# Performance work log

Hardware: AMD Instinct MI355X
Metric: run time of the kernel (lower is better)

The kernel has to match this reference:

```python
import jax, jax.numpy as jnp
import numpy as np
from math import factorial

IRREPS_IN1 = [(128, 0), (64, 1), (32, 2)]  # (mul, l): features
IRREPS_IN2 = [(1, 0), (1, 1), (1, 2)]      # spherical harmonics lmax=2
BATCH = 16384

# ---------- real Clebsch-Gordan coefficients (e3nn convention) ----------

def _su2_cg(j1, j2, j3, m1, m2, m3):
    if m3 != m1 + m2:
        return 0.0
    f = factorial
    pref = ((2 * j3 + 1) * f(j1 + j2 - j3) * f(j1 - j2 + j3) * f(-j1 + j2 + j3) / f(j1 + j2 + j3 + 1)) ** 0.5
    pref *= (f(j3 + m3) * f(j3 - m3) * f(j1 - m1) * f(j1 + m1) * f(j2 - m2) * f(j2 + m2)) ** 0.5
    s = 0.0
    for v in range(0, j1 + j2 - j3 + 1):
        a = j1 + j2 - j3 - v; b = j1 - m1 - v; c = j2 + m2 - v
        d = j3 - j2 + m1 + v; e = j3 - j1 - m2 + v
        if min(a, b, c, d, e) < 0:
            continue
        s += (-1) ** v / (f(v) * f(a) * f(b) * f(c) * f(d) * f(e))
    return pref * s


def _su2_cg_tensor(l1, l2, l3):
    C = np.zeros((2 * l1 + 1, 2 * l2 + 1, 2 * l3 + 1))
    for m1 in range(-l1, l1 + 1):
        for m2 in range(-l2, l2 + 1):
            for m3 in range(-l3, l3 + 1):
                C[l1 + m1, l2 + m2, l3 + m3] = _su2_cg(l1, l2, l3, m1, m2, m3)
    return C


def _q(l):
    # change of basis real -> complex spherical harmonics
    q = np.zeros((2 * l + 1, 2 * l + 1), dtype=np.complex128)
    for m in range(-l, 0):
        q[l + m, l + abs(m)] = 1.0 / np.sqrt(2.0)
        q[l + m, l - abs(m)] = -1j / np.sqrt(2.0)
    q[l, l] = 1.0
    for m in range(1, l + 1):
        q[l + m, l + abs(m)] = (-1) ** m / np.sqrt(2.0)
        q[l + m, l - abs(m)] = 1j * (-1) ** m / np.sqrt(2.0)
    return (-1j) ** l * q


def _real_cg(l1, l2, l3):
    C = _su2_cg_tensor(l1, l2, l3).astype(np.complex128)
    Q1, Q2, Q3 = _q(l1), _q(l2), _q(l3)
    C = np.einsum('ij,kl,mn,ikn->jlm', Q1, Q2, np.conj(Q3.T), C)
    assert np.abs(C.imag).max() < 1e-8
    return np.ascontiguousarray(C.real.astype(np.float32))

# precompute all CG tensors needed by the full tensor product
CG = {}
for _m1, _l1 in IRREPS_IN1:
    for _m2, _l2 in IRREPS_IN2:
        for _l3 in range(abs(_l1 - _l2), _l1 + _l2 + 1):
            if (_l1, _l2, _l3) not in CG:
                CG[(_l1, _l2, _l3)] = _real_cg(_l1, _l2, _l3)


def _tensor_product(x, y):
    """Full CG tensor product. x:[B,480] y:[B,9] -> dict l3 -> list of [B,mul,2l3+1]."""
    B = x.shape[0]
    outs = {}
    off1 = 0
    for mul1, l1 in IRREPS_IN1:
        d1 = 2 * l1 + 1
        x_blk = x[:, off1:off1 + mul1 * d1].reshape(B, mul1, d1)
        off1 += mul1 * d1
        off2 = 0
        for mul2, l2 in IRREPS_IN2:
            d2 = 2 * l2 + 1
            y_blk = y[:, off2:off2 + mul2 * d2].reshape(B, mul2, d2)
            off2 += mul2 * d2
            for l3 in range(abs(l1 - l2), l1 + l2 + 1):
                cg = jnp.asarray(CG[(l1, l2, l3)])  # [d1,d2,d3]
                z = jnp.einsum('ijk,bui,bvj->buvk', cg, x_blk, y_blk)
                outs.setdefault(l3, []).append(z.reshape(B, mul1 * mul2, 2 * l3 + 1))
    return outs


def setup_inputs() -> dict:
    key = jax.random.key(0)
    k = jax.random.split(key, 5)
    dim1 = sum(m * (2 * l + 1) for m, l in IRREPS_IN1)  # 480
    dim2 = sum(m * (2 * l + 1) for m, l in IRREPS_IN2)  # 9
    x = jax.random.normal(k[0], (BATCH, dim1), dtype=jnp.float32)
    y = jax.random.normal(k[1], (BATCH, dim2), dtype=jnp.float32)
    # fan-in per output l of the equivariant Linear (tp outputs with matching l)
    W0 = jax.random.normal(k[2], (224, 128), dtype=jnp.float32)
    W1 = jax.random.normal(k[3], (384, 64), dtype=jnp.float32)
    W2 = jax.random.normal(k[4], (352, 32), dtype=jnp.float32)
    return {"x": x, "y": y, "W0": W0, "W1": W1, "W2": W2}


def reference(x, y, W0, W1, W2):
    B = x.shape[0]
    outs = _tensor_product(x, y)
    Ws = {0: W0, 1: W1, 2: W2}
    res = []
    for mul_out, l in IRREPS_IN1:
        blk = jnp.concatenate(outs[l], axis=1)  # [B, tot_mul, 2l+1]
        tot_mul = blk.shape[1]
        o = jnp.einsum('bui,uv->bvi', blk, Ws[l]) / np.sqrt(tot_mul).astype(np.float32)
        res.append(o.reshape(B, mul_out * (2 * l + 1)))
    return jnp.concatenate(res, axis=1)  # [B, 480]
```

## Files before the change

kernel.cpp:

```cpp
#include <hip/hip_runtime.h>
#include <math.h>
#include <stdint.h>

#define NBATCH 16384
#define MB 16
#define NT 256
#define NBLOCKS (NBATCH/MB)
#define WT_BYTE_OFF 2560

typedef float  f32x4 __attribute__((ext_vector_type(4)));
typedef short  s16x8 __attribute__((ext_vector_type(8)));

constexpr double cfact(int n){ double r=1.0; for(int i=2;i<=n;++i) r*=(double)i; return r; }
constexpr double csqrt_(double x){
  if (x<=0.0) return 0.0;
  double m=x, k=1.0;
  while (m>1.0) { m*=0.25; k*=2.0; }
  while (m<0.25){ m*=4.0;  k*=0.5; }
  double g=0.7;
  for(int i=0;i<14;++i) g = 0.5*(g + m/g);
  return g*k;
}
constexpr double su2d(int j1,int j2,int j3,int m1,int m2,int m3){
  if (m1+m2 != m3) return 0.0;
  double pref = csqrt_((double)(2*j3+1)*cfact(j1+j2-j3)*cfact(j1-j2+j3)*cfact(-j1+j2+j3)/cfact(j1+j2+j3+1));
  pref *= csqrt_(cfact(j3+m3)*cfact(j3-m3)*cfact(j1-m1)*cfact(j1+m1)*cfact(j2-m2)*cfact(j2+m2));
  double s=0.0;
  for (int v=0; v<=j1+j2-j3; ++v){
    int a=j1+j2-j3-v, b=j1-m1-v, c=j2+m2-v, d=j3-j2+m1+v, e=j3-j1-m2+v;
    if (a<0||b<0||c<0||d<0||e<0) continue;
    double t = 1.0/(cfact(v)*cfact(a)*cfact(b)*cfact(c)*cfact(d)*cfact(e));
    s += (v&1)? -t : t;
  }
  return pref*s;
}
struct C2 { double re, im; };
constexpr C2 qvald(int l,int r,int c){
  int m = r - l;
  const double is2 = 0.70710678118654752440;
  double br=0.0, bi=0.0;
  if (m<0){ if (c==l-m) br=is2; else if (c==l+m) bi=-is2; }
  else if (m==0){ if (c==l) br=1.0; }
  else { double sg=(m&1)?-1.0:1.0; if (c==l+m) br=sg*is2; else if (c==l-m) bi=sg*is2; }
  if (l==1){ double nr=bi, ni=-br; br=nr; bi=ni; }
  else if (l==2){ br=-br; bi=-bi; }
  return C2{br,bi};
}
constexpr int HP_L1[15]={0,1,2,0,1,1,1,2,2,0,1,1,2,2,2};
constexpr int HP_L2[15]={0,1,2,1,0,1,2,1,2,2,1,2,0,1,2};
constexpr int HP_L3[15]={0,0,0,1,1,1,1,1,1,2,2,2,2,2,2};
constexpr int HP_CGOFF[15]={0,1,10,35,44,53,80,125,170,245,270,315,390,415,490};
constexpr int HP_TSTART[15]={0,1,4,9,12,21,30,39,54,69,74,89,104,129,154};
constexpr int HP_YOFF[15]={0,1,4,1,0,1,4,1,4,4,1,4,0,1,4};

struct CGT { float v[616]; };
constexpr CGT make_cg_part(int p0, int p1){
  CGT T{};
  for (int z=0; z<616; ++z) T.v[z]=0.f;
  for (int p=p0; p<p1; ++p){
    int l1=HP_L1[p], l2=HP_L2[p], l3=HP_L3[p];
    int d1=2*l1+1, d2=2*l2+1, d3=2*l3+1;
    double su[5][5]={};
    for (int i=0;i<d1;++i) for (int k=0;k<d2;++k){
      int n = i+k-l1-l2+l3;
      su[i][k] = (n>=0 && n<d3) ? su2d(l1,l2,l3, i-l1, k-l2, n-l3) : 0.0;
    }
    for (int i1=0;i1<d1;++i1) for (int i2=0;i2<d2;++i2) for (int i3=0;i3<d3;++i3){
      double val=0.0;
      for (int i=0;i<d1;++i) for (int k=0;k<d2;++k){
        int n = i+k-l1-l2+l3;
        if (n<0||n>=d3) continue;
        double c = su[i][k];
        if (c==0.0) continue;
        C2 q1=qvald(l1,i,i1), q2=qvald(l2,k,i2), q3=qvald(l3,n,i3);
        double ar = q1.re*q2.re - q1.im*q2.im;
        double ai = q1.re*q2.im + q1.im*q2.re;
        val += (ar*q3.re + ai*q3.im)*c;
      }
      T.v[HP_CGOFF[p] + (i1*d2+i2)*d3 + i3] = (float)val;
    }
  }
  return T;
}
constexpr CGT CG_A = make_cg_part(0,8);
constexpr CGT CG_B = make_cg_part(8,12);
constexpr CGT CG_D = make_cg_part(12,15);
constexpr CGT cg_merge(){
  CGT T{};
  for (int i=0;i<616;++i) T.v[i] = CG_A.v[i] + CG_B.v[i] + CG_D.v[i];
  return T;
}
__device__ __constant__ const CGT CGC = cg_merge();

constexpr uint32_t make_td(int e){
  if (e>=179) return 0u;
  int p=0; while (p<14 && e>=HP_TSTART[p+1]) ++p;
  int r = e - HP_TSTART[p];
  int d2 = 2*HP_L2[p]+1, d3 = 2*HP_L3[p]+1;
  int i1 = r/d3, j3 = r - (r/d3)*d3;
  int base = HP_CGOFF[p] + i1*d2*d3 + j3;
  return (uint32_t)base | ((uint32_t)d2<<10) | ((uint32_t)d3<<13) | ((uint32_t)HP_YOFF[p]<<16);
}
struct TDT { uint32_t v[192]; };
constexpr TDT make_tdt(){ TDT t{}; for(int e=0;e<192;++e) t.v[e]=make_td(e); return t; }
__device__ __constant__ const TDT TDC = make_tdt();

constexpr uint16_t cmap1(int o){
  if (o<128) return (uint16_t)o;
  if (o<320){ int s=o-128; int i1=s>>6; int u=s&63; return (uint16_t)(128 + u*3 + i1); }
  if (o<480){ int s=o-320; int i1=s>>5; int u=s&31; return (uint16_t)(320 + u*5 + i1); }
  return (uint16_t)0xFFFF;
}
struct CMT { uint16_t v[512]; };
constexpr CMT make_cm(){ CMT t{}; for(int o=0;o<512;++o) t.v[o]=cmap1(o); return t; }
__device__ __constant__ const CMT CMC = make_cm();

__device__ const int   SEG_WB[15] = {0,16384,24576, 28672,36864,40960,45056,49152,51200,
                                     53248,57344,59392,61440,62464,63488};
__device__ const int   SEG_SH[15] = {7,6,5, 7,6,6,6,5,5, 7,6,6,5,5,5};
__device__ const int   SEG_U0[15] = {0,128,192, 0,128,192,256,320,352, 0,128,192,256,288,320};
__device__ const int   SEG_G[15]  = {0,0,0, 1,1,1,1,1,1, 2,2,2,2,2,2};
__device__ const float SEG_SC[3]  = {0.066815310478f, 0.051031036308f, 0.053300179089f};

__device__ __forceinline__ uint32_t f2bf(float f){
  uint32_t u = __float_as_uint(f);
  return (u + 0x7fffu + ((u>>16)&1u)) >> 16;
}
__device__ __forceinline__ float bf2f(uint32_t v){ return __uint_as_float(v << 16); }

__global__ __launch_bounds__(NT) void pack_w(const float* __restrict__ W0, const float* __restrict__ W1,
                                             const float* __restrict__ W2, float* __restrict__ ws)
{
  int t = blockIdx.x*NT + threadIdx.x;
  uint16_t* wt = (uint16_t*)((char*)ws + WT_BYTE_OFF);
  int j = 0;
  while (j < 14 && t >= SEG_WB[j+1]) ++j;
  int idx = t - SEG_WB[j];
  int sh = SEG_SH[j];
  int v  = idx >> sh, u1 = idx & ((1<<sh)-1);
  int g  = SEG_G[j];
  int N  = (g==0)?128:(g==1)?64:32;
  const float* Wsrc = (g==0)?W0:(g==1)?W1:W2;
  const int vt = v >> 4, ln = v & 15;
  const int kk = u1 >> 5, ko = (u1 >> 3) & 3, s = u1 & 7;
  const int dest = SEG_WB[j] + ((vt << sh) << 4) + kk*512 + (ko*16 + ln)*8 + s;
  wt[dest] = (uint16_t)f2bf(Wsrc[(SEG_U0[j]+u1)*N + v] * SEG_SC[g]);
}

template<int G> struct GM;
template<> struct GM<0>{
  static constexpr int NS=3, D3=1, NMT=2, NI3=1;
  static constexpr int MUL[3]={128,64,32};
  static constexpr int D1[3] ={1,3,5};
  static constexpr int XB[3] ={0,128,320};
  static constexpr int TS[3] ={0,1,4};
  static constexpr int WB[3] ={0,16384,24576};
};
template<> struct GM<1>{
  static constexpr int NS=6, D3=3, NMT=1, NI3=3;
  static constexpr int MUL[6]={128,64,64,64,32,32};
  static constexpr int D1[6] ={1,3,3,3,5,5};
  static constexpr int XB[6] ={0,128,128,128,320,320};
  static constexpr int TS[6] ={9,12,21,30,39,54};
  static constexpr int WB[6] ={28672,36864,40960,45056,49152,51200};
};
template<> struct GM<2>{
  static constexpr int NS=6, D3=5, NMT=1, NI3=3;
  static constexpr int MUL[6]={128,64,64,32,32,32};
  static constexpr int D1[6] ={1,3,3,5,5,5};
  static constexpr int XB[6] ={0,128,128,320,320,320};
  static constexpr int TS[6] ={69,74,89,104,129,154};
  static constexpr int WB[6] ={53248,57344,59392,61440,62464,63488};
};

template<int G, int S, int NMT, int NI3>
__device__ __forceinline__ void do_seg(const short* __restrict__ wt,
                                       const uint16_t* __restrict__ xp,
                                       const uint16_t* __restrict__ Tsh,
                                       f32x4 (&acc)[NMT][NI3],
                                       int lane, int ln, int koct, int mt0, int i3base, int ni3)
{
  using M = GM<G>;
  constexpr int MUL = M::MUL[S];
  constexpr int KS  = MUL >> 5;
  constexpr int D1  = M::D1[S];

  s16x8 Af[NMT][KS];
  const short* wbase = wt + M::WB[S] + lane*8;
  #pragma unroll
  for (int mt = 0; mt < NMT; ++mt)
    #pragma unroll
    for (int kk = 0; kk < KS; ++kk)
      Af[mt][kk] = *(const s16x8*)(wbase + (mt0+mt)*(MUL*16) + kk*512);

  const int swz = (ln & 7) << 4;
  const int koct2 = koct*2;
  const char* xrow = (const char*)xp + ln*1024;

  #pragma unroll
  for (int i1 = 0; i1 < D1; ++i1){
    s16x8 Bf[KS];
    #pragma unroll
    for (int kk = 0; kk < KS; ++kk){
      const int cb = (M::XB[S] + i1*MUL + kk*32)*2 + koct2;
      Bf[kk] = *(const s16x8*)(xrow + (cb ^ swz));
    }
    f32x4 D[NMT];
    #pragma unroll
    for (int mt = 0; mt < NMT; ++mt){
      D[mt] = (f32x4){0.f,0.f,0.f,0.f};
      #pragma unroll
      for (int kk = 0; kk < KS; ++kk)
        D[mt] = __builtin_amdgcn_mfma_f32_16x16x32_bf16(Af[mt][kk], Bf[kk], D[mt], 0, 0, 0);
    }
    #pragma unroll
    for (int j = 0; j < NI3; ++j){
      if (j < ni3){
        const int e = M::TS[S] + i1*M::D3 + i3base + j;
        const float tv = bf2f(Tsh[e*16 + ln]);
        #pragma unroll
        for (int mt = 0; mt < NMT; ++mt){
          acc[mt][j][0] += tv*D[mt][0];
          acc[mt][j][1] += tv*D[mt][1];
          acc[mt][j][2] += tv*D[mt][2];
          acc[mt][j][3] += tv*D[mt][3];
        }
      }
    }
  }
}

template<int G>
__device__ __forceinline__ void run_group(const short* __restrict__ wt,
                                          float* __restrict__ out, int b0, int tid,
                                          const uint16_t* __restrict__ Tsh,
                                          const uint16_t* __restrict__ xp)
{
  using M = GM<G>;
  const int lane = tid & 63, w = tid >> 6;
  const int ln   = lane & 15;
  const int koct = (lane >> 4) * 8;
  constexpr int NMT = M::NMT, NI3 = M::NI3;

  int mt0, i3base, ni3;
  if constexpr (G == 0){ mt0 = 2*w; i3base = 0; ni3 = 1; }
  else if constexpr (G == 1){ mt0 = w; i3base = 0; ni3 = 3; }
  else { mt0 = w >> 1; i3base = (w & 1)*3; ni3 = (w & 1) ? 2 : 3; }

  f32x4 acc[NMT][NI3];
  #pragma unroll
  for (int a = 0; a < NMT; ++a)
    #pragma unroll
    for (int b = 0; b < NI3; ++b) acc[a][b] = (f32x4){0.f,0.f,0.f,0.f};

  do_seg<G,0,NMT,NI3>(wt, xp, Tsh, acc, lane, ln, koct, mt0, i3base, ni3);
  do_seg<G,1,NMT,NI3>(wt, xp, Tsh, acc, lane, ln, koct, mt0, i3base, ni3);
  do_seg<G,2,NMT,NI3>(wt, xp, Tsh, acc, lane, ln, koct, mt0, i3base, ni3);
  if constexpr (M::NS > 3){
    do_seg<G,(M::NS>3)?3:0,NMT,NI3>(wt, xp, Tsh, acc, lane, ln, koct, mt0, i3base, ni3);
    do_seg<G,(M::NS>4)?4:0,NMT,NI3>(wt, xp, Tsh, acc, lane, ln, koct, mt0, i3base, ni3);
    do_seg<G,(M::NS>5)?5:0,NMT,NI3>(wt, xp, Tsh, acc, lane, ln, koct, mt0, i3base, ni3);
  }

  const int rq = (lane >> 4) * 4;
  float* orow = out + (size_t)(b0 + ln)*480;
  if constexpr (G == 0){
    #pragma unroll
    for (int mt = 0; mt < NMT; ++mt){
      const int vb = (mt0+mt)*16 + rq;
      float4 st = make_float4(acc[mt][0][0], acc[mt][0][1], acc[mt][0][2], acc[mt][0][3]);
      *(float4*)(orow + vb) = st;
    }
  } else if constexpr (G == 1){
    const int vb = mt0*16 + rq;
    float buf[12];
    #pragma unroll
    for (int r = 0; r < 4; ++r)
      #pragma unroll
      for (int j = 0; j < 3; ++j) buf[r*3+j] = acc[0][j][r];
    float* p = orow + 128 + vb*3;
    *(float4*)(p)   = make_float4(buf[0],buf[1],buf[2],buf[3]);
    *(float4*)(p+4) = make_float4(buf[4],buf[5],buf[6],buf[7]);
    *(float4*)(p+8) = make_float4(buf[8],buf[9],buf[10],buf[11]);
  } else {
    const int vb = mt0*16 + rq;
    #pragma unroll
    for (int r = 0; r < 4; ++r)
      #pragma unroll
      for (int j = 0; j < 3; ++j)
        if (j < ni3)
          orow[320 + (vb+r)*5 + i3base + j] = acc[0][j][r];
  }
}

__global__ __launch_bounds__(NT) void tp_fused(const float* __restrict__ x,
                                               const float* __restrict__ y,
                                               const float* __restrict__ ws,
                                               float* __restrict__ out)
{
  __shared__ __align__(16) uint16_t xs[MB*480];
  __shared__ __align__(16) uint16_t xp[MB*512];
  __shared__ __align__(16) uint16_t Tsh[192*16];

  const int tid = threadIdx.x;
  const int b0 = blockIdx.x * MB;
  const short* wt = (const short*)((const char*)ws + WT_BYTE_OFF);
  const int w = tid >> 6, l = tid & 63;
  const int r0 = 4*w;

  {
    const float4* src = (const float4*)(x + (size_t)(b0 + r0)*480);
    uint16_t* xsb = xs + r0*480;
    #pragma unroll
    for (int it = 0; it < 8; ++it){
      const int i = it*64 + l;
      if (it < 7 || i < 480){
        float4 v = src[i];
        uint16_t p[4] = {(uint16_t)f2bf(v.x),(uint16_t)f2bf(v.y),
                         (uint16_t)f2bf(v.z),(uint16_t)f2bf(v.w)};
        *(uint2*)(&xsb[i*4]) = *(const uint2*)p;
      }
    }
  }

  if (tid < 179){
    const uint32_t td = TDC.v[tid];
    const int base = td & 1023, d2 = (td>>10)&7, str = (td>>13)&7, yoff = (td>>16)&7;
    const float* yb = y + (size_t)b0*9 + yoff;
    uint16_t tv[16];
    #pragma unroll
    for (int b = 0; b < 16; ++b){
      float t = 0.f;
      for (int i2 = 0; i2 < d2; ++i2) t += CGC.v[base + i2*str] * yb[b*9 + i2];
      tv[b] = (uint16_t)f2bf(t);
    }
    *(uint4*)(&Tsh[tid*16])     = *(const uint4*)&tv[0];
    *(uint4*)(&Tsh[tid*16 + 8]) = *(const uint4*)&tv[8];
  }

  {
    const uint4 m4 = ((const uint4*)CMC.v)[l];
    const uint16_t* mp = (const uint16_t*)&m4;
    #pragma unroll
    for (int r = 0; r < 4; ++r){
      const int row = r0 + r;
      const uint16_t* xsr = xs + row*480;
      uint16_t vals[8];
      #pragma unroll
      for (int jj = 0; jj < 8; ++jj){
        const uint16_t c = mp[jj];
        vals[jj] = (c == 0xFFFFu) ? (uint16_t)0 : xsr[c];
      }
      *(uint4*)((char*)xp + row*1024 + ((l*16) ^ ((row&7)<<4))) = *(const uint4*)vals;
    }
  }
  __syncthreads();

  run_group<0>(wt, out, b0, tid, Tsh, xp);
  run_group<1>(wt, out, b0, tid, Tsh, xp);
  run_group<2>(wt, out, b0, tid, Tsh, xp);
}

extern "C" void kernel_launch(void* const* d_in, const int* in_sizes, int n_in,
                              void* d_out, int out_size, void* d_ws, size_t ws_size,
                              hipStream_t stream)
{
  const float* x  = (const float*)d_in[0];
  const float* y  = (const float*)d_in[1];
  const float* W0 = (const float*)d_in[2];
  const float* W1 = (const float*)d_in[3];
  const float* W2 = (const float*)d_in[4];
  float* out = (float*)d_out;
  float* ws  = (float*)d_ws;

  hipLaunchKernelGGL(pack_w, dim3(252), dim3(NT), 0, stream, W0, W1, W2, ws);
  hipLaunchKernelGGL(tp_fused, dim3(NBLOCKS), dim3(NT), 0, stream, x, y, ws, out);
}
```

Before: 121.3 us.

## Double batch tile to 32 rows with 512 threads, splitting waves across batch tiles

New measurement: 141.8 us. 1.17x slower.

```diff
diff --git a/kernel.cpp b/kernel.cpp
--- a/kernel.cpp
+++ b/kernel.cpp
@@ -3,8 +3,8 @@
 #include <stdint.h>
 
 #define NBATCH 16384
-#define MB 16
-#define NT 256
+#define MB 32
+#define NT 512
 #define NBLOCKS (NBATCH/MB)
 #define WT_BYTE_OFF 2560
 
@@ -128,10 +128,10 @@
 }
 __device__ __forceinline__ float bf2f(uint32_t v){ return __uint_as_float(v << 16); }
 
-__global__ __launch_bounds__(NT) void pack_w(const float* __restrict__ W0, const float* __restrict__ W1,
-                                             const float* __restrict__ W2, float* __restrict__ ws)
-{
-  int t = blockIdx.x*NT + threadIdx.x;
+__global__ __launch_bounds__(256) void pack_w(const float* __restrict__ W0, const float* __restrict__ W1,
+                                              const float* __restrict__ W2, float* __restrict__ ws)
+{
+  int t = blockIdx.x*256 + threadIdx.x;
   uint16_t* wt = (uint16_t*)((char*)ws + WT_BYTE_OFF);
   int j = 0;
   while (j < 14 && t >= SEG_WB[j+1]) ++j;
@@ -149,7 +149,7 @@
 
 template<int G> struct GM;
 template<> struct GM<0>{
-  static constexpr int NS=3, D3=1, NMT=2, NI3=1;
+  static constexpr int NS=3, D3=1;
   static constexpr int MUL[3]={128,64,32};
   static constexpr int D1[3] ={1,3,5};
   static constexpr int XB[3] ={0,128,320};
@@ -157,7 +157,7 @@
   static constexpr int WB[3] ={0,16384,24576};
 };
 template<> struct GM<1>{
-  static constexpr int NS=6, D3=3, NMT=1, NI3=3;
+  static constexpr int NS=6, D3=3;
   static constexpr int MUL[6]={128,64,64,64,32,32};
   static constexpr int D1[6] ={1,3,3,3,5,5};
   static constexpr int XB[6] ={0,128,128,128,320,320};
@@ -165,7 +165,7 @@
   static constexpr int WB[6] ={28672,36864,40960,45056,49152,51200};
 };
 template<> struct GM<2>{
-  static constexpr int NS=6, D3=5, NMT=1, NI3=3;
+  static constexpr int NS=6, D3=5;
   static constexpr int MUL[6]={128,64,64,32,32,32};
   static constexpr int D1[6] ={1,3,3,5,5,5};
   static constexpr int XB[6] ={0,128,128,320,320,320};
@@ -173,57 +173,53 @@
   static constexpr int WB[6] ={53248,57344,59392,61440,62464,63488};
 };
 
-template<int G, int S, int NMT, int NI3>
+template<int G, int S, int TILES, int NI3>
 __device__ __forceinline__ void do_seg(const short* __restrict__ wt,
                                        const uint16_t* __restrict__ xp,
                                        const uint16_t* __restrict__ Tsh,
-                                       f32x4 (&acc)[NMT][NI3],
-                                       int lane, int ln, int koct, int mt0, int i3base, int ni3)
+                                       f32x4 (&acc)[TILES][NI3],
+                                       int lane, int ln, int koct,
+                                       int mt0, int tbase, int i3base, int ni3)
 {
   using M = GM<G>;
   constexpr int MUL = M::MUL[S];
   constexpr int KS  = MUL >> 5;
   constexpr int D1  = M::D1[S];
 
-  s16x8 Af[NMT][KS];
-  const short* wbase = wt + M::WB[S] + lane*8;
+  s16x8 Af[KS];
+  const short* wbase = wt + M::WB[S] + lane*8 + mt0*(MUL*16);
   #pragma unroll
-  for (int mt = 0; mt < NMT; ++mt)
-    #pragma unroll
-    for (int kk = 0; kk < KS; ++kk)
-      Af[mt][kk] = *(const s16x8*)(wbase + (mt0+mt)*(MUL*16) + kk*512);
+  for (int kk = 0; kk < KS; ++kk)
+    Af[kk] = *(const s16x8*)(wbase + kk*512);
 
   const int swz = (ln & 7) << 4;
   const int koct2 = koct*2;
-  const char* xrow = (const char*)xp + ln*1024;
 
   #pragma unroll
   for (int i1 = 0; i1 < D1; ++i1){
-    s16x8 Bf[KS];
-    #pragma unroll
-    for (int kk = 0; kk < KS; ++kk){
-      const int cb = (M::XB[S] + i1*MUL + kk*32)*2 + koct2;
-      Bf[kk] = *(const s16x8*)(xrow + (cb ^ swz));
-    }
-    f32x4 D[NMT];
-    #pragma unroll
-    for (int mt = 0; mt < NMT; ++mt){
-      D[mt] = (f32x4){0.f,0.f,0.f,0.f};
+    #pragma unroll
+    for (int t = 0; t < TILES; ++t){
+      const int row = (tbase + t)*16 + ln;
+      const char* xrow = (const char*)xp + row*1024;
+      s16x8 Bf[KS];
+      #pragma unroll
+      for (int kk = 0; kk < KS; ++kk){
+        const int cb = (M::XB[S] + i1*MUL + kk*32)*2 + koct2;
+        Bf[kk] = *(const s16x8*)(xrow + (cb ^ swz));
+      }
+      f32x4 D = {0.f,0.f,0.f,0.f};
       #pragma unroll
       for (int kk = 0; kk < KS; ++kk)
-        D[mt] = __builtin_amdgcn_mfma_f32_16x16x32_bf16(Af[mt][kk], Bf[kk], D[mt], 0, 0, 0);
-    }
-    #pragma unroll
-    for (int j = 0; j < NI3; ++j){
-      if (j < ni3){
-        const int e = M::TS[S] + i1*M::D3 + i3base + j;
-        const float tv = bf2f(Tsh[e*16 + ln]);
-        #pragma unroll
-        for (int mt = 0; mt < NMT; ++mt){
-          acc[mt][j][0] += tv*D[mt][0];
-          acc[mt][j][1] += tv*D[mt][1];
-          acc[mt][j][2] += tv*D[mt][2];
-          acc[mt][j][3] += tv*D[mt][3];
+        D = __builtin_amdgcn_mfma_f32_16x16x32_bf16(Af[kk], Bf[kk], D, 0, 0, 0);
+      #pragma unroll
+      for (int j = 0; j < NI3; ++j){
+        if (j < ni3){
+          const int e = M::TS[S] + i1*M::D3 + i3base + j;
+          const float tv = bf2f(Tsh[e*32 + row]);
+          acc[t][j][0] += tv*D[0];
+          acc[t][j][1] += tv*D[1];
+          acc[t][j][2] += tv*D[2];
+          acc[t][j][3] += tv*D[3];
         }
       }
     }
@@ -240,38 +236,40 @@
   const int lane = tid & 63, w = tid >> 6;
   const int ln   = lane & 15;
   const int koct = (lane >> 4) * 8;
-  constexpr int NMT = M::NMT, NI3 = M::NI3;
-
-  int mt0, i3base, ni3;
-  if constexpr (G == 0){ mt0 = 2*w; i3base = 0; ni3 = 1; }
-  else if constexpr (G == 1){ mt0 = w; i3base = 0; ni3 = 3; }
-  else { mt0 = w >> 1; i3base = (w & 1)*3; ni3 = (w & 1) ? 2 : 3; }
-
-  f32x4 acc[NMT][NI3];
+  constexpr int TILES = (G == 0) ? 2 : 1;
+  constexpr int NI3   = (G == 0) ? 1 : 3;
+
+  int mt0, tbase, i3base, ni3;
+  if constexpr (G == 0){ mt0 = w;        tbase = 0;     i3base = 0;        ni3 = 1; }
+  else if constexpr (G == 1){ mt0 = w&3; tbase = w>>2;  i3base = 0;        ni3 = 3; }
+  else { mt0 = (w>>1)&1;                 tbase = w>>2;  i3base = (w&1)*3;  ni3 = (w&1) ? 2 : 3; }
+
+  f32x4 acc[TILES][NI3];
   #pragma unroll
-  for (int a = 0; a < NMT; ++a)
+  for (int a = 0; a < TILES; ++a)
     #pragma unroll
     for (int b = 0; b < NI3; ++b) acc[a][b] = (f32x4){0.f,0.f,0.f,0.f};
 
-  do_seg<G,0,NMT,NI3>(wt, xp, Tsh, acc, lane, ln, koct, mt0, i3base, ni3);
-  do_seg<G,1,NMT,NI3>(wt, xp, Tsh, acc, lane, ln, koct, mt0, i3base, ni3);
-  do_seg<G,2,NMT,NI3>(wt, xp, Tsh, acc, lane, ln, koct, mt0, i3base, ni3);
+  do_seg<G,0,TILES,NI3>(wt, xp, Tsh, acc, lane, ln, koct, mt0, tbase, i3base, ni3);
+  do_seg<G,1,TILES,NI3>(wt, xp, Tsh, acc, lane, ln, koct, mt0, tbase, i3base, ni3);
+  do_seg<G,2,TILES,NI3>(wt, xp, Tsh, acc, lane, ln, koct, mt0, tbase, i3base, ni3);
   if constexpr (M::NS > 3){
-    do_seg<G,(M::NS>3)?3:0,NMT,NI3>(wt, xp, Tsh, acc, lane, ln, koct, mt0, i3base, ni3);
-    do_seg<G,(M::NS>4)?4:0,NMT,NI3>(wt, xp, Tsh, acc, lane, ln, koct, mt0, i3base, ni3);
-    do_seg<G,(M::NS>5)?5:0,NMT,NI3>(wt, xp, Tsh, acc, lane, ln, koct, mt0, i3base, ni3);
+    do_seg<G,(M::NS>3)?3:0,TILES,NI3>(wt, xp, Tsh, acc, lane, ln, koct, mt0, tbase, i3base, ni3);
+    do_seg<G,(M::NS>4)?4:0,TILES,NI3>(wt, xp, Tsh, acc, lane, ln, koct, mt0, tbase, i3base, ni3);
+    do_seg<G,(M::NS>5)?5:0,TILES,NI3>(wt, xp, Tsh, acc, lane, ln, koct, mt0, tbase, i3base, ni3);
   }
 
   const int rq = (lane >> 4) * 4;
-  float* orow = out + (size_t)(b0 + ln)*480;
   if constexpr (G == 0){
     #pragma unroll
-    for (int mt = 0; mt < NMT; ++mt){
-      const int vb = (mt0+mt)*16 + rq;
-      float4 st = make_float4(acc[mt][0][0], acc[mt][0][1], acc[mt][0][2], acc[mt][0][3]);
+    for (int t = 0; t < 2; ++t){
+      float* orow = out + (size_t)(b0 + t*16 + ln)*480;
+      const int vb = mt0*16 + rq;
+      float4 st = make_float4(acc[t][0][0], acc[t][0][1], acc[t][0][2], acc[t][0][3]);
       *(float4*)(orow + vb) = st;
     }
   } else if constexpr (G == 1){
+    float* orow = out + (size_t)(b0 + tbase*16 + ln)*480;
     const int vb = mt0*16 + rq;
     float buf[12];
     #pragma unroll
@@ -283,6 +281,7 @@
     *(float4*)(p+4) = make_float4(buf[4],buf[5],buf[6],buf[7]);
     *(float4*)(p+8) = make_float4(buf[8],buf[9],buf[10],buf[11]);
   } else {
+    float* orow = out + (size_t)(b0 + tbase*16 + ln)*480;
     const int vb = mt0*16 + rq;
     #pragma unroll
     for (int r = 0; r < 4; ++r)
@@ -293,14 +292,14 @@
   }
 }
 
-__global__ __launch_bounds__(NT) void tp_fused(const float* __restrict__ x,
-                                               const float* __restrict__ y,
-                                               const float* __restrict__ ws,
-                                               float* __restrict__ out)
+__global__ __launch_bounds__(NT, 4) void tp_fused(const float* __restrict__ x,
+                                                  const float* __restrict__ y,
+                                                  const float* __restrict__ ws,
+                                                  float* __restrict__ out)
 {
   __shared__ __align__(16) uint16_t xs[MB*480];
   __shared__ __align__(16) uint16_t xp[MB*512];
-  __shared__ __align__(16) uint16_t Tsh[192*16];
+  __shared__ __align__(16) uint16_t Tsh[192*32];
 
   const int tid = threadIdx.x;
   const int b0 = blockIdx.x * MB;
@@ -323,10 +322,11 @@
     }
   }
 
-  if (tid < 179){
-    const uint32_t td = TDC.v[tid];
+  if (tid < 358){
+    const int e = tid >> 1, half = tid & 1;
+    const uint32_t td = TDC.v[e];
     const int base = td & 1023, d2 = (td>>10)&7, str = (td>>13)&7, yoff = (td>>16)&7;
-    const float* yb = y + (size_t)b0*9 + yoff;
+    const float* yb = y + (size_t)(b0 + half*16)*9 + yoff;
     uint16_t tv[16];
     #pragma unroll
     for (int b = 0; b < 16; ++b){
@@ -334,8 +334,9 @@
       for (int i2 = 0; i2 < d2; ++i2) t += CGC.v[base + i2*str] * yb[b*9 + i2];
       tv[b] = (uint16_t)f2bf(t);
     }
-    *(uint4*)(&Tsh[tid*16])     = *(const uint4*)&tv[0];
-    *(uint4*)(&Tsh[tid*16 + 8]) = *(const uint4*)&tv[8];
+    uint16_t* dst = &Tsh[e*32 + half*16];
+    *(uint4*)(dst)     = *(const uint4*)&tv[0];
+    *(uint4*)(dst + 8) = *(const uint4*)&tv[8];
   }
 
   {
@@ -373,6 +374,6 @@
   float* out = (float*)d_out;
   float* ws  = (float*)d_ws;
 
-  hipLaunchKernelGGL(pack_w, dim3(252), dim3(NT), 0, stream, W0, W1, W2, ws);
+  hipLaunchKernelGGL(pack_w, dim3(252), dim3(256), 0, stream, W0, W1, W2, ws);
   hipLaunchKernelGGL(tp_fused, dim3(NBLOCKS), dim3(NT), 0, stream, x, y, ws, out);
 }
```

## Drop staging LDS buffer and split G0 tiles to raise occupancy

Applied to the files above, without the earlier changes.

Result: slower. 184.0 us (+51.7%).

```diff
diff --git a/kernel.cpp b/kernel.cpp
--- a/kernel.cpp
+++ b/kernel.cpp
@@ -128,10 +128,10 @@
 }
 __device__ __forceinline__ float bf2f(uint32_t v){ return __uint_as_float(v << 16); }
 
-__global__ __launch_bounds__(NT) void pack_w(const float* __restrict__ W0, const float* __restrict__ W1,
-                                             const float* __restrict__ W2, float* __restrict__ ws)
-{
-  int t = blockIdx.x*NT + threadIdx.x;
+__global__ __launch_bounds__(256) void pack_w(const float* __restrict__ W0, const float* __restrict__ W1,
+                                              const float* __restrict__ W2, float* __restrict__ ws)
+{
+  int t = blockIdx.x*256 + threadIdx.x;
   uint16_t* wt = (uint16_t*)((char*)ws + WT_BYTE_OFF);
   int j = 0;
   while (j < 14 && t >= SEG_WB[j+1]) ++j;
@@ -149,7 +149,7 @@
 
 template<int G> struct GM;
 template<> struct GM<0>{
-  static constexpr int NS=3, D3=1, NMT=2, NI3=1;
+  static constexpr int NS=3, D3=1;
   static constexpr int MUL[3]={128,64,32};
   static constexpr int D1[3] ={1,3,5};
   static constexpr int XB[3] ={0,128,320};
@@ -157,7 +157,7 @@
   static constexpr int WB[3] ={0,16384,24576};
 };
 template<> struct GM<1>{
-  static constexpr int NS=6, D3=3, NMT=1, NI3=3;
+  static constexpr int NS=6, D3=3;
   static constexpr int MUL[6]={128,64,64,64,32,32};
   static constexpr int D1[6] ={1,3,3,3,5,5};
   static constexpr int XB[6] ={0,128,128,128,320,320};
@@ -165,7 +165,7 @@
   static constexpr int WB[6] ={28672,36864,40960,45056,49152,51200};
 };
 template<> struct GM<2>{
-  static constexpr int NS=6, D3=5, NMT=1, NI3=3;
+  static constexpr int NS=6, D3=5;
   static constexpr int MUL[6]={128,64,64,32,32,32};
   static constexpr int D1[6] ={1,3,3,5,5,5};
   static constexpr int XB[6] ={0,128,128,320,320,320};
@@ -173,11 +173,11 @@
   static constexpr int WB[6] ={53248,57344,59392,61440,62464,63488};
 };
 
-template<int G, int S, int NMT, int NI3>
+template<int G, int S, int NI3>
 __device__ __forceinline__ void do_seg(const short* __restrict__ wt,
                                        const uint16_t* __restrict__ xp,
                                        const uint16_t* __restrict__ Tsh,
-                                       f32x4 (&acc)[NMT][NI3],
+                                       f32x4 (&acc)[NI3],
                                        int lane, int ln, int koct, int mt0, int i3base, int ni3)
 {
   using M = GM<G>;
@@ -185,13 +185,11 @@
   constexpr int KS  = MUL >> 5;
   constexpr int D1  = M::D1[S];
 
-  s16x8 Af[NMT][KS];
-  const short* wbase = wt + M::WB[S] + lane*8;
+  s16x8 Af[KS];
+  const short* wbase = wt + M::WB[S] + lane*8 + mt0*(MUL*16);
   #pragma unroll
-  for (int mt = 0; mt < NMT; ++mt)
-    #pragma unroll
-    for (int kk = 0; kk < KS; ++kk)
-      Af[mt][kk] = *(const s16x8*)(wbase + (mt0+mt)*(MUL*16) + kk*512);
+  for (int kk = 0; kk < KS; ++kk)
+    Af[kk] = *(const s16x8*)(wbase + kk*512);
 
   const int swz = (ln & 7) << 4;
   const int koct2 = koct*2;
@@ -205,26 +203,19 @@
       const int cb = (M::XB[S] + i1*MUL + kk*32)*2 + koct2;
       Bf[kk] = *(const s16x8*)(xrow + (cb ^ swz));
     }
-    f32x4 D[NMT];
-    #pragma unroll
-    for (int mt = 0; mt < NMT; ++mt){
-      D[mt] = (f32x4){0.f,0.f,0.f,0.f};
-      #pragma unroll
-      for (int kk = 0; kk < KS; ++kk)
-        D[mt] = __builtin_amdgcn_mfma_f32_16x16x32_bf16(Af[mt][kk], Bf[kk], D[mt], 0, 0, 0);
-    }
+    f32x4 D = {0.f,0.f,0.f,0.f};
+    #pragma unroll
+    for (int kk = 0; kk < KS; ++kk)
+      D = __builtin_amdgcn_mfma_f32_16x16x32_bf16(Af[kk], Bf[kk], D, 0, 0, 0);
     #pragma unroll
     for (int j = 0; j < NI3; ++j){
       if (j < ni3){
         const int e = M::TS[S] + i1*M::D3 + i3base + j;
         const float tv = bf2f(Tsh[e*16 + ln]);
-        #pragma unroll
-        for (int mt = 0; mt < NMT; ++mt){
-          acc[mt][j][0] += tv*D[mt][0];
-          acc[mt][j][1] += tv*D[mt][1];
-          acc[mt][j][2] += tv*D[mt][2];
-          acc[mt][j][3] += tv*D[mt][3];
-        }
+        acc[j][0] += tv*D[0];
+        acc[j][1] += tv*D[1];
+        acc[j][2] += tv*D[2];
+        acc[j][3] += tv*D[3];
       }
     }
   }
@@ -240,65 +231,71 @@
   const int lane = tid & 63, w = tid >> 6;
   const int ln   = lane & 15;
   const int koct = (lane >> 4) * 8;
-  constexpr int NMT = M::NMT, NI3 = M::NI3;
-
-  int mt0, i3base, ni3;
-  if constexpr (G == 0){ mt0 = 2*w; i3base = 0; ni3 = 1; }
-  else if constexpr (G == 1){ mt0 = w; i3base = 0; ni3 = 3; }
-  else { mt0 = w >> 1; i3base = (w & 1)*3; ni3 = (w & 1) ? 2 : 3; }
-
-  f32x4 acc[NMT][NI3];
-  #pragma unroll
-  for (int a = 0; a < NMT; ++a)
-    #pragma unroll
-    for (int b = 0; b < NI3; ++b) acc[a][b] = (f32x4){0.f,0.f,0.f,0.f};
-
-  do_seg<G,0,NMT,NI3>(wt, xp, Tsh, acc, lane, ln, koct, mt0, i3base, ni3);
-  do_seg<G,1,NMT,NI3>(wt, xp, Tsh, acc, lane, ln, koct, mt0, i3base, ni3);
-  do_seg<G,2,NMT,NI3>(wt, xp, Tsh, acc, lane, ln, koct, mt0, i3base, ni3);
-  if constexpr (M::NS > 3){
-    do_seg<G,(M::NS>3)?3:0,NMT,NI3>(wt, xp, Tsh, acc, lane, ln, koct, mt0, i3base, ni3);
-    do_seg<G,(M::NS>4)?4:0,NMT,NI3>(wt, xp, Tsh, acc, lane, ln, koct, mt0, i3base, ni3);
-    do_seg<G,(M::NS>5)?5:0,NMT,NI3>(wt, xp, Tsh, acc, lane, ln, koct, mt0, i3base, ni3);
-  }
-
-  const int rq = (lane >> 4) * 4;
+  const int rq   = (lane >> 4) * 4;
   float* orow = out + (size_t)(b0 + ln)*480;
+
   if constexpr (G == 0){
-    #pragma unroll
-    for (int mt = 0; mt < NMT; ++mt){
-      const int vb = (mt0+mt)*16 + rq;
-      float4 st = make_float4(acc[mt][0][0], acc[mt][0][1], acc[mt][0][2], acc[mt][0][3]);
+    #pragma unroll 1
+    for (int mt = 0; mt < 2; ++mt){
+      const int m0 = 2*w + mt;
+      f32x4 acc[1];
+      acc[0] = (f32x4){0.f,0.f,0.f,0.f};
+      do_seg<0,0,1>(wt, xp, Tsh, acc, lane, ln, koct, m0, 0, 1);
+      do_seg<0,1,1>(wt, xp, Tsh, acc, lane, ln, koct, m0, 0, 1);
+      do_seg<0,2,1>(wt, xp, Tsh, acc, lane, ln, koct, m0, 0, 1);
+      const int vb = m0*16 + rq;
+      float4 st = make_float4(acc[0][0], acc[0][1], acc[0][2], acc[0][3]);
       *(float4*)(orow + vb) = st;
     }
   } else if constexpr (G == 1){
+    const int mt0 = w;
+    f32x4 acc[3];
+    #pragma unroll
+    for (int b = 0; b < 3; ++b) acc[b] = (f32x4){0.f,0.f,0.f,0.f};
+    do_seg<1,0,3>(wt, xp, Tsh, acc, lane, ln, koct, mt0, 0, 3);
+    do_seg<1,1,3>(wt, xp, Tsh, acc, lane, ln, koct, mt0, 0, 3);
+    do_seg<1,2,3>(wt, xp, Tsh, acc, lane, ln, koct, mt0, 0, 3);
+    do_seg<1,3,3>(wt, xp, Tsh, acc, lane, ln, koct, mt0, 0, 3);
+    do_seg<1,4,3>(wt, xp, Tsh, acc, lane, ln, koct, mt0, 0, 3);
+    do_seg<1,5,3>(wt, xp, Tsh, acc, lane, ln, koct, mt0, 0, 3);
     const int vb = mt0*16 + rq;
     float buf[12];
     #pragma unroll
     for (int r = 0; r < 4; ++r)
       #pragma unroll
-      for (int j = 0; j < 3; ++j) buf[r*3+j] = acc[0][j][r];
+      for (int j = 0; j < 3; ++j) buf[r*3+j] = acc[j][r];
     float* p = orow + 128 + vb*3;
     *(float4*)(p)   = make_float4(buf[0],buf[1],buf[2],buf[3]);
     *(float4*)(p+4) = make_float4(buf[4],buf[5],buf[6],buf[7]);
     *(float4*)(p+8) = make_float4(buf[8],buf[9],buf[10],buf[11]);
   } else {
+    const int mt0 = w >> 1;
+    const int i3base = (w & 1)*3;
+    const int ni3 = (w & 1) ? 2 : 3;
+    f32x4 acc[3];
+    #pragma unroll
+    for (int b = 0; b < 3; ++b) acc[b] = (f32x4){0.f,0.f,0.f,0.f};
+    do_seg<2,0,3>(wt, xp, Tsh, acc, lane, ln, koct, mt0, i3base, ni3);
+    do_seg<2,1,3>(wt, xp, Tsh, acc, lane, ln, koct, mt0, i3base, ni3);
+    do_seg<2,2,3>(wt, xp, Tsh, acc, lane, ln, koct, mt0, i3base, ni3);
+    do_seg<2,3,3>(wt, xp, Tsh, acc, lane, ln, koct, mt0, i3base, ni3);
+    do_seg<2,4,3>(wt, xp, Tsh, acc, lane, ln, koct, mt0, i3base, ni3);
+    do_seg<2,5,3>(wt, xp, Tsh, acc, lane, ln, koct, mt0, i3base, ni3);
     const int vb = mt0*16 + rq;
     #pragma unroll
     for (int r = 0; r < 4; ++r)
       #pragma unroll
       for (int j = 0; j < 3; ++j)
         if (j < ni3)
-          orow[320 + (vb+r)*5 + i3base + j] = acc[0][j][r];
-  }
-}
-
-__global__ __launch_bounds__(NT) void tp_fused(const float* __restrict__ x,
-                                               const float* __restrict__ y,
-                                               const float* __restrict__ ws,
-                                               float* __restrict__ out)
-{
-  __shared__ __align__(16) uint16_t xs[MB*480];
+          orow[320 + (vb+r)*5 + i3base + j] = acc[j][r];
+  }
+}
+
+__global__ __launch_bounds__(NT, 5) void tp_fused(const float* __restrict__ x,
+                                                  const float* __restrict__ y,
+                                                  const float* __restrict__ ws,
+                                                  float* __restrict__ out)
+{
   __shared__ __align__(16) uint16_t xp[MB*512];
   __shared__ __align__(16) uint16_t Tsh[192*16];
 
@@ -310,15 +307,15 @@
 
   {
     const float4* src = (const float4*)(x + (size_t)(b0 + r0)*480);
-    uint16_t* xsb = xs + r0*480;
     #pragma unroll
     for (int it = 0; it < 8; ++it){
       const int i = it*64 + l;
       if (it < 7 || i < 480){
         float4 v = src[i];
+        const int r = i/120, cc = i - r*120;
         uint16_t p[4] = {(uint16_t)f2bf(v.x),(uint16_t)f2bf(v.y),
                          (uint16_t)f2bf(v.z),(uint16_t)f2bf(v.w)};
-        *(uint2*)(&xsb[i*4]) = *(const uint2*)p;
+        *(uint2*)(&xp[(r0 + r)*512 + cc*4]) = *(const uint2*)p;
       }
     }
   }
@@ -344,7 +341,7 @@
     #pragma unroll
     for (int r = 0; r < 4; ++r){
       const int row = r0 + r;
-      const uint16_t* xsr = xs + row*480;
+      const uint16_t* xsr = xp + row*512;
       uint16_t vals[8];
       #pragma unroll
       for (int jj = 0; jj < 8; ++jj){
@@ -373,6 +370,6 @@
   float* out = (float*)d_out;
   float* ws  = (float*)d_ws;
 
-  hipLaunchKernelGGL(pack_w, dim3(252), dim3(NT), 0, stream, W0, W1, W2, ws);
+  hipLaunchKernelGGL(pack_w, dim3(252), dim3(256), 0, stream, W0, W1, W2, ws);
   hipLaunchKernelGGL(tp_fused, dim3(NBLOCKS), dim3(NT), 0, stream, x, y, ws, out);
 }
```
